# Kernel tuning notes

Hardware: AMD Instinct MI355X
Metric: run time of the kernel (lower is better)

## Reference

```python
import jax, jax.numpy as jnp
import numpy as np

B, CIN, COUT, K, H, W = 8, 512, 512, 3, 64, 64
SCALE = 1.0 / np.sqrt(CIN * K * K).astype(np.float32)  # conv.scale
LRELU_SCALE = 1.4142135623730951  # sqrt(2), FusedLeakyReLU scale


def setup_inputs() -> dict:
    key = jax.random.key(0)
    ks = jax.random.split(key, 6)
    return {
        "x": jax.random.normal(ks[0], (B, CIN, H, W), jnp.float32),
        "style": jax.random.normal(ks[1], (B, CIN), jnp.float32),
        "noise": jax.random.normal(ks[2], (1, 1, H, W), jnp.float32),
        "weight": jax.random.normal(ks[3], (COUT, CIN, K, K), jnp.float32),
        "bias": jnp.zeros((COUT,), jnp.float32),
        "noise_strength": jax.random.uniform(ks[4], (1,), jnp.float32),
    }


def reference(x, style, noise, weight, bias, noise_strength):
    # Modulate: scale * weight * style  -> [B, Cout, Cin, K, K]
    w = SCALE * weight[None] * style[:, None, :, None, None]
    # Demodulate per (batch, out_channel)
    demod = jax.lax.rsqrt(jnp.sum(w * w, axis=(2, 3, 4)) + 1e-8)
    w = w * demod[:, :, None, None, None]
    # Per-sample conv (grouped-conv trick in torch) via vmap over batch
    pad = K // 2
    def conv_one(xi, wi):  # xi: [Cin,H,W], wi: [Cout,Cin,K,K]
        return jax.lax.conv_general_dilated(
            xi[None], wi, window_strides=(1, 1),
            padding=[(pad, pad), (pad, pad)],
            dimension_numbers=("NCHW", "OIHW", "NCHW"))[0]
    out = jax.vmap(conv_one)(x, w)  # [B, Cout, H, W]
    # NoiseInjection: out + strength * noise (noise broadcast over B, C)
    out = out + noise_strength[0] * noise
    # FusedLeakyReLU: leaky_relu(out + bias, 0.2) * sqrt(2)
    y = out + bias[None, :, None, None]
    return jnp.where(y >= 0, y, 0.2 * y) * LRELU_SCALE
```

## Files before the change

### kernel.cpp

```cpp
#include <hip/hip_runtime.h>
#include <hip/hip_bf16.h>

typedef __attribute__((ext_vector_type(8))) short s16x8;
typedef __attribute__((ext_vector_type(16))) float f32x16;

#define MOD_SCALE 0.014731391274719739f

__device__ __forceinline__ void gload_lds16(const void* g, void* l) {
    __builtin_amdgcn_global_load_lds(
        (const __attribute__((address_space(1))) unsigned int*)g,
        (__attribute__((address_space(3))) unsigned int*)l, 16, 0, 0);
}

__device__ __forceinline__ void sync_drain() {
    __builtin_amdgcn_s_waitcnt(0);
    __syncthreads();
}

__global__ __launch_bounds__(256) void k_prep(const float* __restrict__ x,
                                              const float* __restrict__ style,
                                              const float* __restrict__ weight,
                                              __hip_bfloat16* __restrict__ xs,
                                              __hip_bfloat16* __restrict__ wb,
                                              float* __restrict__ dem) {
    __shared__ __align__(16) char sm[36864];
    const int t = threadIdx.x;
    const int bid = blockIdx.x;

    if (bid < 512) {
        const int b = bid >> 6, h = bid & 63;
        __hip_bfloat16 (*tile)[68] = (__hip_bfloat16(*)[68])sm;
        float* sf = (float*)(sm + 17408);
        sf[t] = style[b * 512 + t] * MOD_SCALE;
        sf[t + 256] = style[b * 512 + 256 + t] * MOD_SCALE;
        const float* xb = x + (size_t)b * 512 * 4096 + h * 64;
        const int cig = t & 3, w = t >> 2;
        char* ob = (char*)xs + (size_t)b * 4460544 +
                   (size_t)((h + 1) * 66 + 1) * 64;
        __syncthreads();
#pragma unroll
        for (int cq = 0; cq < 4; ++cq) {
#pragma unroll 4
            for (int it = 0; it < 8; ++it) {
                int idx = it * 256 + t;
                int cil = idx >> 4, w4 = idx & 15;
                int ci = cq * 128 + cil;
                float4 v = *(const float4*)(xb + (size_t)ci * 4096 + w4 * 4);
                float s = sf[ci];
                union { uint2 u2; __hip_bfloat16 q[4]; } pk;
                pk.q[0] = __float2bfloat16(v.x * s);
                pk.q[1] = __float2bfloat16(v.y * s);
                pk.q[2] = __float2bfloat16(v.z * s);
                pk.q[3] = __float2bfloat16(v.w * s);
                *(uint2*)&tile[cil][w4 * 4] = pk.u2;
            }
            __syncthreads();
#pragma unroll
            for (int cbl = 0; cbl < 4; ++cbl) {
                const int cb = cq * 4 + cbl;
                union { uint4 u; __hip_bfloat16 q[8]; } pk;
#pragma unroll
                for (int j = 0; j < 8; ++j)
                    pk.q[j] = tile[cbl * 32 + cig * 8 + j][w];
                *(uint4*)(ob + (size_t)cb * 278784 + w * 64 + cig * 16) = pk.u;
            }
            __syncthreads();
        }
    } else if (bid < 1032) {
        const int idx = (bid - 512) * 256 + t;
        const int b = idx / 16640;
        const int r2 = idx - b * 16640;
        const int cb = r2 / 1040;
        const int r3 = r2 - cb * 1040;
        const int pair = r3 >> 2;
        const int chunk = r3 & 3;
        int pr, pc;
        if (pair < 66)       { pr = 0;          pc = pair; }
        else if (pair < 132) { pr = 65;         pc = pair - 66; }
        else if (pair < 196) { pr = pair - 131; pc = 0; }
        else                 { pr = pair - 195; pc = 65; }
        char* d = (char*)xs +
                  ((size_t)(b * 16 + cb) * 4356 + pr * 66 + pc) * 64 +
                  chunk * 16;
        *(uint4*)d = make_uint4(0u, 0u, 0u, 0u);
    } else if (bid < 1288) {
        const int r = bid - 1032;
        float* lds = (float*)sm;
        const int p0 = r * 1024;
        const float* src = weight + (size_t)p0 * 9;
#pragma unroll
        for (int k = 0; k < 36; ++k) lds[k * 256 + t] = src[k * 256 + t];
        __syncthreads();
#pragma unroll
        for (int tap = 0; tap < 9; ++tap) {
            union { uint2 u; __hip_bfloat16 q[4]; } pk;
#pragma unroll
            for (int j = 0; j < 4; ++j)
                pk.q[j] = __float2bfloat16(lds[(4 * t + j) * 9 + tap]);
            *(uint2*)(wb + (size_t)tap * 262144 + p0 + 4 * t) = pk.u;
        }
    } else {
        const int co = bid - 1288;
        float* s2 = (float*)sm;
        for (int i = t; i < 4096; i += 256) { float v = style[i]; s2[i] = v * v; }
        __syncthreads();
        const float4* wp = (const float4*)(weight + (size_t)co * 4608);
        float acc[8] = {0.f, 0.f, 0.f, 0.f, 0.f, 0.f, 0.f, 0.f};
        for (int j = t; j < 1152; j += 256) {
            float4 v = wp[j];
            float w2[4] = {v.x * v.x, v.y * v.y, v.z * v.z, v.w * v.w};
            int base = j * 4;
#pragma unroll
            for (int e = 0; e < 4; ++e) {
                int ci = (base + e) / 9;
                float ww = w2[e];
#pragma unroll
                for (int bb = 0; bb < 8; ++bb) acc[bb] += ww * s2[bb * 512 + ci];
            }
        }
#pragma unroll
        for (int bb = 0; bb < 8; ++bb)
            for (int off = 32; off > 0; off >>= 1)
                acc[bb] += __shfl_down(acc[bb], off);
        float* red = (float*)(sm + 16384);
        const int wv = t >> 6, lane = t & 63;
        if (lane == 0) {
#pragma unroll
            for (int bb = 0; bb < 8; ++bb) red[wv * 8 + bb] = acc[bb];
        }
        __syncthreads();
        if (t < 8) {
            float s = red[t] + red[8 + t] + red[16 + t] + red[24 + t];
            const float S2 = MOD_SCALE * MOD_SCALE;
            dem[t * 512 + co] = rsqrtf(S2 * s + 1e-8f);
        }
    }
}

__global__ __launch_bounds__(256, 2) void k_conv(
    const __hip_bfloat16* __restrict__ xs,
    const __hip_bfloat16* __restrict__ wb,
    const float* __restrict__ demod,
    const float* __restrict__ noise,
    const float* __restrict__ bias,
    const float* __restrict__ nstr,
    float* __restrict__ out) {
    __shared__ __align__(16) char Xl[25344];
    __shared__ __align__(16) char Wl[6][8192];

    const int t = threadIdx.x;
    const int bi = blockIdx.x;
    const int spat = bi & 127;
    const int b = spat >> 4;
    const int h0 = (spat & 15) << 2;
    const int co0 = (bi >> 7) << 7;
    const int lane = t & 63;
    const int wv = t >> 6;
    const int wm = wv & 1, wn = wv >> 1;
    const int el = lane & 31;
    const int hk = lane >> 5;

    f32x16 acc[2][4];
#pragma unroll
    for (int i = 0; i < 2; ++i)
#pragma unroll
        for (int j = 0; j < 4; ++j)
#pragma unroll
            for (int k = 0; k < 16; ++k) acc[i][j][k] = 0.f;

    const char* xsb = (const char*)xs + (size_t)b * 4460544;
    const char* xsrc[7];
#pragma unroll
    for (int i = 0; i < 6; ++i) {
        int g = i * 256 + t;
        int e = g >> 2, s = g & 3;
        int gc = (s - (e >> 2)) & 3;
        int row = e / 66, col = e - row * 66;
        xsrc[i] = xsb + (size_t)((h0 + row) * 66 + col) * 64 + gc * 16;
    }
    {
        int g = 1536 + t;
        int e = g >> 2, s = g & 3;
        int gc = (s - (e >> 2)) & 3;
        int row = e / 66, col = e - row * 66;
        xsrc[6] = xsb + (size_t)((h0 + row) * 66 + col) * 64 + gc * 16;
    }
    const char* wsrc[2];
#pragma unroll
    for (int i = 0; i < 2; ++i) {
        int g = i * 256 + t;
        int e = g >> 2, s = g & 3;
        int gc = (s - (e >> 2)) & 3;
        wsrc[i] = (const char*)wb + (size_t)(co0 + e) * 1024 + gc * 16;
    }
    const int wvoff = wv << 10;

#pragma unroll
    for (int i = 0; i < 6; ++i) gload_lds16(xsrc[i], Xl + i * 4096 + wvoff);
    if (t < 48) gload_lds16(xsrc[6], Xl + 24576);
#pragma unroll
    for (int tt = 0; tt < 3; ++tt)
#pragma unroll
        for (int i = 0; i < 2; ++i)
            gload_lds16(wsrc[i] + (size_t)tt * 524288,
                        Wl[tt] + i * 4096 + wvoff);
    sync_drain();

    int cboff = 0;
    for (int cb = 0; cb < 16; ++cb, cboff += 64) {
        const int ncboff = (cb < 15) ? cboff + 64 : cboff;
#pragma unroll
        for (int p = 0; p < 3; ++p) {
            const int bank = ((cb + p) & 1) * 3;
            const int nbank = 3 - bank;
#pragma unroll
            for (int tt = 0; tt < 3; ++tt) {
                const size_t soff = (p < 2)
                    ? (size_t)(3 * (p + 1) + tt) * 524288 + cboff
                    : (size_t)tt * 524288 + ncboff;
                char* dst = Wl[nbank + tt] + wvoff;
#pragma unroll
                for (int i = 0; i < 2; ++i)
                    gload_lds16(wsrc[i] + soff, dst + i * 4096);
            }
#pragma unroll
            for (int tt = 0; tt < 3; ++tt) {
                const char* Wb = Wl[bank + tt];
#pragma unroll
                for (int ks = 0; ks < 2; ++ks) {
                    const int c = 2 * ks + hk;
                    s16x8 af[2], bfr[4];
#pragma unroll
                    for (int mi = 0; mi < 2; ++mi) {
                        int e = wm * 64 + mi * 32 + el;
                        af[mi] = *(const s16x8*)(Wb + e * 64 +
                                                 (((c + (e >> 2)) & 3) << 4));
                    }
#pragma unroll
                    for (int ni = 0; ni < 4; ++ni) {
                        int e = (2 * wn + (ni >> 1) + p) * 66 + tt +
                                (ni & 1) * 32 + el;
                        bfr[ni] = *(const s16x8*)(Xl + e * 64 +
                                                  (((c + (e >> 2)) & 3) << 4));
                    }
#pragma unroll
                    for (int mi = 0; mi < 2; ++mi)
#pragma unroll
                        for (int ni = 0; ni < 4; ++ni)
                            acc[mi][ni] =
                                __builtin_amdgcn_mfma_f32_32x32x16_bf16(
                                    af[mi], bfr[ni], acc[mi][ni], 0, 0, 0);
                }
            }
            sync_drain();
        }
        if (cb < 15) {
            const size_t xo = (size_t)(cb + 1) * 278784;
#pragma unroll
            for (int i = 0; i < 6; ++i)
                gload_lds16(xsrc[i] + xo, Xl + i * 4096 + wvoff);
            if (t < 48) gload_lds16(xsrc[6] + xo, Xl + 24576);
            sync_drain();
        }
    }

    const float nsv = nstr[0];
    const float LR = 1.4142135623730951f;
#pragma unroll
    for (int mi = 0; mi < 2; ++mi) {
        float dm[16], bs[16];
#pragma unroll
        for (int rg = 0; rg < 16; ++rg) {
            int co = co0 + wm * 64 + mi * 32 + (rg & 3) + 8 * (rg >> 2) + 4 * hk;
            dm[rg] = demod[b * 512 + co];
            bs[rg] = bias[co];
        }
#pragma unroll
        for (int ni = 0; ni < 4; ++ni) {
            int h = h0 + 2 * wn + (ni >> 1);
            int w = (ni & 1) * 32 + el;
            float nz = nsv * noise[h * 64 + w];
#pragma unroll
            for (int rg = 0; rg < 16; ++rg) {
                int co = co0 + wm * 64 + mi * 32 + (rg & 3) + 8 * (rg >> 2) +
                         4 * hk;
                float v = acc[mi][ni][rg] * dm[rg] + nz + bs[rg];
                v = (v >= 0.f ? v : 0.2f * v) * LR;
                out[(((size_t)b * 512 + co) * 64 + h) * 64 + w] = v;
            }
        }
    }
}

extern "C" void kernel_launch(void* const* d_in, const int* in_sizes, int n_in,
                              void* d_out, int out_size, void* d_ws, size_t ws_size,
                              hipStream_t stream) {
    const float* x      = (const float*)d_in[0];
    const float* style  = (const float*)d_in[1];
    const float* noise  = (const float*)d_in[2];
    const float* weight = (const float*)d_in[3];
    const float* bias   = (const float*)d_in[4];
    const float* nstr   = (const float*)d_in[5];
    float* out = (float*)d_out;

    char* ws = (char*)d_ws;
    __hip_bfloat16* xs = (__hip_bfloat16*)ws;
    __hip_bfloat16* wb = (__hip_bfloat16*)(ws + 35684352);
    float* demod = (float*)(ws + 35684352 + 4718592);

    k_prep<<<1800, 256, 0, stream>>>(x, style, weight, xs, wb, demod);
    k_conv<<<512, 256, 0, stream>>>(xs, wb, demod, noise, bias, nstr, out);
}
```

Baseline: 254.9 us.

## Shrink conv tiles to two waves and stream weights one tap at a time

Halves the conv block to 128 threads covering two output rows and 128 output channels, doubling the grid to 1024 blocks. Weight staging changes from triple-tap groups in six LDS buffers to single taps in a double buffer, cutting LDS use per block. This aims to raise occupancy and improve load balance across CUs. The tradeoff is more input halo reloaded per output and three times as many barriers per channel block.

```diff
diff --git a/kernel.cpp b/kernel.cpp
--- a/kernel.cpp
+++ b/kernel.cpp
@@ -137,7 +137,7 @@
     }
 }
 
-__global__ __launch_bounds__(256, 2) void k_conv(
+__global__ __launch_bounds__(128, 2) void k_conv(
     const __hip_bfloat16* __restrict__ xs,
     const __hip_bfloat16* __restrict__ wb,
     const float* __restrict__ demod,
@@ -145,18 +145,17 @@
     const float* __restrict__ bias,
     const float* __restrict__ nstr,
     float* __restrict__ out) {
-    __shared__ __align__(16) char Xl[25344];
-    __shared__ __align__(16) char Wl[6][8192];
+    __shared__ __align__(16) char Xl[16896];
+    __shared__ __align__(16) char Wl[2][8192];
 
     const int t = threadIdx.x;
     const int bi = blockIdx.x;
-    const int spat = bi & 127;
-    const int b = spat >> 4;
-    const int h0 = (spat & 15) << 2;
-    const int co0 = (bi >> 7) << 7;
+    const int spat = bi & 255;
+    const int b = spat >> 5;
+    const int h0 = (spat & 31) << 1;
+    const int co0 = (bi >> 8) << 7;
     const int lane = t & 63;
     const int wv = t >> 6;
-    const int wm = wv & 1, wn = wv >> 1;
     const int el = lane & 31;
     const int hk = lane >> 5;
 
@@ -169,26 +168,26 @@
             for (int k = 0; k < 16; ++k) acc[i][j][k] = 0.f;
 
     const char* xsb = (const char*)xs + (size_t)b * 4460544;
-    const char* xsrc[7];
-#pragma unroll
-    for (int i = 0; i < 6; ++i) {
-        int g = i * 256 + t;
+    const char* xsrc[9];
+#pragma unroll
+    for (int i = 0; i < 8; ++i) {
+        int g = i * 128 + t;
         int e = g >> 2, s = g & 3;
         int gc = (s - (e >> 2)) & 3;
         int row = e / 66, col = e - row * 66;
         xsrc[i] = xsb + (size_t)((h0 + row) * 66 + col) * 64 + gc * 16;
     }
     {
-        int g = 1536 + t;
+        int g = 1024 + t;
         int e = g >> 2, s = g & 3;
         int gc = (s - (e >> 2)) & 3;
         int row = e / 66, col = e - row * 66;
-        xsrc[6] = xsb + (size_t)((h0 + row) * 66 + col) * 64 + gc * 16;
-    }
-    const char* wsrc[2];
-#pragma unroll
-    for (int i = 0; i < 2; ++i) {
-        int g = i * 256 + t;
+        xsrc[8] = xsb + (size_t)((h0 + row) * 66 + col) * 64 + gc * 16;
+    }
+    const char* wsrc[4];
+#pragma unroll
+    for (int i = 0; i < 4; ++i) {
+        int g = i * 128 + t;
         int e = g >> 2, s = g & 3;
         int gc = (s - (e >> 2)) & 3;
         wsrc[i] = (const char*)wb + (size_t)(co0 + e) * 1024 + gc * 16;
@@ -196,70 +195,63 @@
     const int wvoff = wv << 10;
 
 #pragma unroll
-    for (int i = 0; i < 6; ++i) gload_lds16(xsrc[i], Xl + i * 4096 + wvoff);
-    if (t < 48) gload_lds16(xsrc[6], Xl + 24576);
-#pragma unroll
-    for (int tt = 0; tt < 3; ++tt)
-#pragma unroll
-        for (int i = 0; i < 2; ++i)
-            gload_lds16(wsrc[i] + (size_t)tt * 524288,
-                        Wl[tt] + i * 4096 + wvoff);
+    for (int i = 0; i < 8; ++i) gload_lds16(xsrc[i], Xl + i * 2048 + wvoff);
+    if (t < 32) gload_lds16(xsrc[8], Xl + 16384);
+#pragma unroll
+    for (int i = 0; i < 4; ++i)
+        gload_lds16(wsrc[i], Wl[0] + i * 2048 + wvoff);
     sync_drain();
 
     int cboff = 0;
     for (int cb = 0; cb < 16; ++cb, cboff += 64) {
-        const int ncboff = (cb < 15) ? cboff + 64 : cboff;
-#pragma unroll
-        for (int p = 0; p < 3; ++p) {
-            const int bank = ((cb + p) & 1) * 3;
-            const int nbank = 3 - bank;
-#pragma unroll
-            for (int tt = 0; tt < 3; ++tt) {
-                const size_t soff = (p < 2)
-                    ? (size_t)(3 * (p + 1) + tt) * 524288 + cboff
-                    : (size_t)tt * 524288 + ncboff;
-                char* dst = Wl[nbank + tt] + wvoff;
-#pragma unroll
-                for (int i = 0; i < 2; ++i)
-                    gload_lds16(wsrc[i] + soff, dst + i * 4096);
-            }
-#pragma unroll
-            for (int tt = 0; tt < 3; ++tt) {
-                const char* Wb = Wl[bank + tt];
-#pragma unroll
-                for (int ks = 0; ks < 2; ++ks) {
-                    const int c = 2 * ks + hk;
-                    s16x8 af[2], bfr[4];
-#pragma unroll
-                    for (int mi = 0; mi < 2; ++mi) {
-                        int e = wm * 64 + mi * 32 + el;
-                        af[mi] = *(const s16x8*)(Wb + e * 64 +
-                                                 (((c + (e >> 2)) & 3) << 4));
-                    }
-#pragma unroll
-                    for (int ni = 0; ni < 4; ++ni) {
-                        int e = (2 * wn + (ni >> 1) + p) * 66 + tt +
-                                (ni & 1) * 32 + el;
-                        bfr[ni] = *(const s16x8*)(Xl + e * 64 +
-                                                  (((c + (e >> 2)) & 3) << 4));
-                    }
-#pragma unroll
-                    for (int mi = 0; mi < 2; ++mi)
-#pragma unroll
-                        for (int ni = 0; ni < 4; ++ni)
-                            acc[mi][ni] =
-                                __builtin_amdgcn_mfma_f32_32x32x16_bf16(
-                                    af[mi], bfr[ni], acc[mi][ni], 0, 0, 0);
+#pragma unroll
+        for (int tap = 0; tap < 9; ++tap) {
+            const int buf = (cb + tap) & 1;
+            if (tap < 8) {
+                char* Wn = Wl[buf ^ 1];
+#pragma unroll
+                for (int i = 0; i < 4; ++i)
+                    gload_lds16(wsrc[i] + (size_t)(tap + 1) * 524288 + cboff,
+                                Wn + i * 2048 + wvoff);
+            } else if (cb < 15) {
+                char* Wn = Wl[buf ^ 1];
+#pragma unroll
+                for (int i = 0; i < 4; ++i)
+                    gload_lds16(wsrc[i] + cboff + 64, Wn + i * 2048 + wvoff);
+            }
+            const int dh = tap / 3, dw = tap % 3;
+            const char* Wb = Wl[buf];
+#pragma unroll
+            for (int ks = 0; ks < 2; ++ks) {
+                const int c = 2 * ks + hk;
+                s16x8 af[2], bfr[4];
+#pragma unroll
+                for (int mi = 0; mi < 2; ++mi) {
+                    int e = wv * 64 + mi * 32 + el;
+                    af[mi] = *(const s16x8*)(Wb + e * 64 +
+                                             (((c + (e >> 2)) & 3) << 4));
                 }
+#pragma unroll
+                for (int ni = 0; ni < 4; ++ni) {
+                    int e = ((ni >> 1) + dh) * 66 + dw + (ni & 1) * 32 + el;
+                    bfr[ni] = *(const s16x8*)(Xl + e * 64 +
+                                              (((c + (e >> 2)) & 3) << 4));
+                }
+#pragma unroll
+                for (int mi = 0; mi < 2; ++mi)
+#pragma unroll
+                    for (int ni = 0; ni < 4; ++ni)
+                        acc[mi][ni] = __builtin_amdgcn_mfma_f32_32x32x16_bf16(
+                            af[mi], bfr[ni], acc[mi][ni], 0, 0, 0);
             }
             sync_drain();
         }
         if (cb < 15) {
             const size_t xo = (size_t)(cb + 1) * 278784;
 #pragma unroll
-            for (int i = 0; i < 6; ++i)
-                gload_lds16(xsrc[i] + xo, Xl + i * 4096 + wvoff);
-            if (t < 48) gload_lds16(xsrc[6] + xo, Xl + 24576);
+            for (int i = 0; i < 8; ++i)
+                gload_lds16(xsrc[i] + xo, Xl + i * 2048 + wvoff);
+            if (t < 32) gload_lds16(xsrc[8] + xo, Xl + 16384);
             sync_drain();
         }
     }
@@ -271,18 +263,18 @@
         float dm[16], bs[16];
 #pragma unroll
         for (int rg = 0; rg < 16; ++rg) {
-            int co = co0 + wm * 64 + mi * 32 + (rg & 3) + 8 * (rg >> 2) + 4 * hk;
+            int co = co0 + wv * 64 + mi * 32 + (rg & 3) + 8 * (rg >> 2) + 4 * hk;
             dm[rg] = demod[b * 512 + co];
             bs[rg] = bias[co];
         }
 #pragma unroll
         for (int ni = 0; ni < 4; ++ni) {
-            int h = h0 + 2 * wn + (ni >> 1);
+            int h = h0 + (ni >> 1);
             int w = (ni & 1) * 32 + el;
             float nz = nsv * noise[h * 64 + w];
 #pragma unroll
             for (int rg = 0; rg < 16; ++rg) {
-                int co = co0 + wm * 64 + mi * 32 + (rg & 3) + 8 * (rg >> 2) +
+                int co = co0 + wv * 64 + mi * 32 + (rg & 3) + 8 * (rg >> 2) +
                          4 * hk;
                 float v = acc[mi][ni][rg] * dm[rg] + nz + bs[rg];
                 v = (v >= 0.f ? v : 0.2f * v) * LR;
@@ -309,5 +301,5 @@
     float* demod = (float*)(ws + 35684352 + 4718592);
 
     k_prep<<<1800, 256, 0, stream>>>(x, style, weight, xs, wb, demod);
-    k_conv<<<512, 256, 0, stream>>>(xs, wb, demod, noise, bias, nstr, out);
-}
+    k_conv<<<1024, 128, 0, stream>>>(xs, wb, demod, noise, bias, nstr, out);
+}
```

Result: slower. 276.8 us (+8.6%).
